# Performance work log

Measured on AMD Instinct MI355X. Metric: run time of the kernel, lower is better.

## Reference

```python
import jax, jax.numpy as jnp
import numpy as np

N_E = 8192
E_DIM = 256
BETA = 0.25


def setup_inputs() -> dict:
    key = jax.random.key(0)
    k1, k2 = jax.random.split(key)
    z = jax.random.normal(k1, (8, E_DIM, 32, 32), dtype=jnp.float32)
    # nn.Embedding default init: N(0, 1)
    W = jax.random.normal(k2, (N_E, E_DIM), dtype=jnp.float32)
    return {"z": z, "W": W}


def reference(z, W):
    # logits: (B, n_e, H, W)
    logits = jnp.einsum('bdhw,nd->bnhw', z, W)
    soft_one_hot = jax.nn.softmax(logits, axis=1)
    ind = jnp.argmax(soft_one_hot, axis=1)  # (B, H, W)
    hard_one_hot = jax.nn.one_hot(ind, N_E, axis=1, dtype=logits.dtype)  # (B, n_e, H, W)
    # straight-through estimator
    one_hot = hard_one_hot - jax.lax.stop_gradient(soft_one_hot) + soft_one_hot
    z_q = jnp.einsum('bnhw,nd->bdhw', one_hot, W)
    z_q_2 = jnp.einsum('bnhw,nd->bdhw', hard_one_hot, W)
    quant_loss = (jnp.mean((z_q - z) ** 2)
                  + jnp.mean((jax.lax.stop_gradient(z_q_2) - z) ** 2)
                  + BETA * jnp.mean((z_q_2 - jax.lax.stop_gradient(z)) ** 2))
    ind_flat = jnp.reshape(ind, (-1,))
    return z_q, quant_loss, ind_flat
```

## Files before the change

kernel.cpp:

```cpp
#include <hip/hip_runtime.h>
#include <math.h>


using short8  = __attribute__((ext_vector_type(8))) short;
using floatx4 = __attribute__((ext_vector_type(4))) float;

#define MARGIN 0.5f
#define APAD   264

__device__ inline unsigned short f2bf(float x) {
    union { float f; unsigned u; } v; v.f = x;
    unsigned r = v.u + 0x7fffu + ((v.u >> 16) & 1u);
    return (unsigned short)(r >> 16);
}

__global__ void conv_w_kernel(const float* __restrict__ W, unsigned short* __restrict__ wb) {
    int i = blockIdx.x * 256 + threadIdx.x;
    float4 v = *(const float4*)&W[(size_t)i * 4];
    ushort4 o;
    o.x = f2bf(v.x); o.y = f2bf(v.y); o.z = f2bf(v.z); o.w = f2bf(v.w);
    *(ushort4*)&wb[(size_t)i * 4] = o;
}

__global__ void conv_z_kernel(const float* __restrict__ z, unsigned short* __restrict__ zb) {
    __shared__ float tile[64 * 65];
    int b  = blockIdx.x >> 6;
    int dt = (blockIdx.x >> 4) & 3;
    int st = blockIdx.x & 15;
    int dl = threadIdx.x >> 6, sl = threadIdx.x & 63;
#pragma unroll
    for (int i = 0; i < 16; ++i) {
        int d = i * 4 + dl;
        tile[sl * 65 + d] = z[(size_t)b * 262144 + (size_t)(dt * 64 + d) * 1024 + st * 64 + sl];
    }
    __syncthreads();
    int d2 = threadIdx.x & 63, sr = threadIdx.x >> 6;
#pragma unroll
    for (int i = 0; i < 16; ++i) {
        int s = i * 4 + sr;
        int pos = b * 1024 + st * 64 + s;
        zb[(size_t)pos * 256 + dt * 64 + d2] = f2bf(tile[s * 65 + d2]);
    }
}

__global__ __launch_bounds__(256, 2)
void gemm_argmax_kernel(const unsigned short* __restrict__ zb,
                        const unsigned short* __restrict__ wb,
                        float4* __restrict__ part)
{
    __shared__ unsigned short As[128 * APAD];
    __shared__ unsigned short Bs[128 * 32];

    const int t  = threadIdx.x;
    const int bm = blockIdx.x, bn = blockIdx.y;
    const int w  = t >> 6, lane = t & 63;
    const int wm = w >> 1, wn = w & 1;
    const int q  = lane >> 4, l15 = lane & 15;

    {
        const unsigned short* src = zb + (size_t)bm * 128 * 256;
#pragma unroll
        for (int i = 0; i < 16; ++i) {
            int u = i * 256 + t;
            int row = u >> 5, c8 = (u & 31) * 8;
            short8 v = *(const short8*)(src + row * 256 + c8);
            *(short8*)(&As[row * APAD + c8]) = v;
        }
    }

    float mv[4][4];
    int   mi[4][4];
#pragma unroll
    for (int im = 0; im < 4; ++im)
#pragma unroll
        for (int r = 0; r < 4; ++r) { mv[im][r] = -INFINITY; mi[im][r] = 0; }

    const unsigned short* wsrc = wb + (size_t)bn * 1024 * 256;

    for (int nc = 0; nc < 8; ++nc) {
        floatx4 acc[4][4];
#pragma unroll
        for (int im = 0; im < 4; ++im)
#pragma unroll
            for (int in = 0; in < 4; ++in) {
                floatx4 zz = {0.f, 0.f, 0.f, 0.f};
                acc[im][in] = zz;
            }

        for (int kp = 0; kp < 8; ++kp) {
            __syncthreads();
#pragma unroll
            for (int i = 0; i < 2; ++i) {
                int u = i * 256 + t;
                int row = u >> 2, q2 = u & 3;
                int ksw = (q2 ^ ((row >> 1) & 3)) * 8;
                const unsigned short* g = wsrc + (size_t)(nc * 128 + row) * 256 + kp * 32 + ksw;
                __builtin_amdgcn_global_load_lds(
                    (const __attribute__((address_space(1))) void*)g,
                    (__attribute__((address_space(3))) void*)(&Bs[u * 8]),
                    16, 0, 0);
            }
            __syncthreads();

            short8 af[4], bf[4];
#pragma unroll
            for (int im = 0; im < 4; ++im)
                af[im] = *(const short8*)(&As[(wm * 64 + im * 16 + l15) * APAD + kp * 32 + q * 8]);
#pragma unroll
            for (int in = 0; in < 4; ++in) {
                int n32 = wn * 64 + in * 16 + l15;
                bf[in] = *(const short8*)(&Bs[n32 * 32 + (q ^ ((n32 >> 1) & 3)) * 8]);
            }
#pragma unroll
            for (int im = 0; im < 4; ++im)
#pragma unroll
                for (int in = 0; in < 4; ++in)
                    acc[im][in] = __builtin_amdgcn_mfma_f32_16x16x32_bf16(
                        af[im], bf[in], acc[im][in], 0, 0, 0);
        }

#pragma unroll
        for (int im = 0; im < 4; ++im)
#pragma unroll
            for (int in = 0; in < 4; ++in) {
                int n = bn * 1024 + nc * 128 + wn * 64 + in * 16 + l15;
#pragma unroll
                for (int r = 0; r < 4; ++r) {
                    float v = acc[im][in][r];
                    if (v > mv[im][r]) { mv[im][r] = v; mi[im][r] = n; }
                }
            }
    }

#pragma unroll
    for (int im = 0; im < 4; ++im)
#pragma unroll
        for (int r = 0; r < 4; ++r) {
            float v1 = mv[im][r]; int i1 = mi[im][r];
            float v2 = -INFINITY; int i2 = 0x7FFFFFFF;
#pragma unroll
            for (int off = 1; off < 16; off <<= 1) {
                float o1 = __shfl_xor(v1, off, 64); int oi1 = __shfl_xor(i1, off, 64);
                float o2 = __shfl_xor(v2, off, 64); int oi2 = __shfl_xor(i2, off, 64);
                if (o1 > v1 || (o1 == v1 && oi1 < i1)) {
                    float tv = v1; int ti = i1; v1 = o1; i1 = oi1;
                    if (tv > o2 || (tv == o2 && ti < oi2)) { o2 = tv; oi2 = ti; }
                }
                if (o2 > v2 || (o2 == v2 && oi2 < i2)) { v2 = o2; i2 = oi2; }
            }
            if (l15 == 0) {
                int pos = bm * 128 + wm * 64 + im * 16 + q * 4 + r;
                float4 rec;
                rec.x = v1; rec.y = __int_as_float(i1);
                rec.z = v2; rec.w = __int_as_float(i2);
                part[(size_t)pos * 16 + bn * 2 + wn] = rec;
            }
        }
}

__global__ __launch_bounds__(256, 8)
void resolve_kernel(const float* __restrict__ z, const float* __restrict__ W,
                    const float4* __restrict__ part,
                    float* __restrict__ zq, float* __restrict__ loss,
                    float* __restrict__ ind)
{
    __shared__ float lred[4];
    const int t = threadIdx.x, w = t >> 6, lane = t & 63;
    const int p = blockIdx.x * 4 + w;
    const int b = p >> 10, s = p & 1023;

    const float* zp = z + (size_t)b * 262144 + s;
    float zf0 = zp[(size_t)(lane * 4 + 0) * 1024];
    float zf1 = zp[(size_t)(lane * 4 + 1) * 1024];
    float zf2 = zp[(size_t)(lane * 4 + 2) * 1024];
    float zf3 = zp[(size_t)(lane * 4 + 3) * 1024];

    float4 rec = part[(size_t)p * 16 + (lane & 15)];
    float vmax = fmaxf(rec.x, rec.z);
#pragma unroll
    for (int off = 1; off < 64; off <<= 1)
        vmax = fmaxf(vmax, __shfl_xor(vmax, off, 64));
    const float thr = vmax - MARGIN;

    int cloc = ((lane < 16) ? ((rec.x >= thr) ? 1 : 0) + ((rec.z >= thr) ? 1 : 0) : 0);
#pragma unroll
    for (int off = 1; off < 64; off <<= 1) cloc += __shfl_xor(cloc, off, 64);
    const int cnt = cloc;

    int bi;
    if (cnt <= 1) {
        float bv = -INFINITY; bi = 0x7FFFFFFF;
#pragma unroll
        for (int s16 = 0; s16 < 16; ++s16) {
            float v1 = __shfl(rec.x, s16, 64); int i1 = __float_as_int(__shfl(rec.y, s16, 64));
            float v2 = __shfl(rec.z, s16, 64); int i2 = __float_as_int(__shfl(rec.w, s16, 64));
            if (v1 > bv || (v1 == bv && i1 < bi)) { bv = v1; bi = i1; }
            if (v2 > bv || (v2 == bv && i2 < bi)) { bv = v2; bi = i2; }
        }
    } else {
        float bv = -INFINITY; bi = 0x7FFFFFFF;
#pragma unroll
        for (int s16 = 0; s16 < 16; ++s16) {
            float vv[2]; int ii[2];
            vv[0] = __shfl(rec.x, s16, 64); ii[0] = __float_as_int(__shfl(rec.y, s16, 64));
            vv[1] = __shfl(rec.z, s16, 64); ii[1] = __float_as_int(__shfl(rec.w, s16, 64));
#pragma unroll
            for (int h = 0; h < 2; ++h) {
                if (vv[h] < thr) continue;
                int c = ii[h];
                float4 wf = *(const float4*)&W[(size_t)c * 256 + lane * 4];
                float d = zf0 * wf.x + zf1 * wf.y + zf2 * wf.z + zf3 * wf.w;
#pragma unroll
                for (int off = 1; off < 64; off <<= 1) d += __shfl_xor(d, off, 64);
                if (d > bv || (d == bv && c < bi)) { bv = d; bi = c; }
            }
        }
    }

    if (lane == 0) ind[p] = (float)bi;

    float4 wq = *(const float4*)&W[(size_t)bi * 256 + lane * 4];
    float* zqp = zq + (size_t)b * 262144 + s;
    zqp[(size_t)(lane * 4 + 0) * 1024] = wq.x;
    zqp[(size_t)(lane * 4 + 1) * 1024] = wq.y;
    zqp[(size_t)(lane * 4 + 2) * 1024] = wq.z;
    zqp[(size_t)(lane * 4 + 3) * 1024] = wq.w;

    float d0 = wq.x - zf0, d1 = wq.y - zf1, d2 = wq.z - zf2, d3 = wq.w - zf3;
    float ls = d0 * d0 + d1 * d1 + d2 * d2 + d3 * d3;
#pragma unroll
    for (int off = 1; off < 64; off <<= 1) ls += __shfl_xor(ls, off, 64);
    if (lane == 0) lred[w] = ls;
    __syncthreads();
    if (t == 0)
        atomicAdd(loss, (lred[0] + lred[1] + lred[2] + lred[3]) * (2.25f / 2097152.0f));
}

#define TP 16
#define ZPAD 260
#define WPAD 36
__global__ __launch_bounds__(256, 2)
void vq_kernel(const float* __restrict__ z, const float* __restrict__ W,
               float* __restrict__ zq, float* __restrict__ loss,
               float* __restrict__ ind)
{
    __shared__ float zs[TP * ZPAD];
    __shared__ float ws[256 * WPAD];
    __shared__ int   best[TP];
    __shared__ float lred[4];
    const int t = threadIdx.x, w = t >> 6, lane = t & 63, cg = t & 63;
    const int pos_base = blockIdx.x * TP;
    const int b = pos_base >> 10, s0 = pos_base & 1023;
    const float* zb = z + (size_t)b * 262144 + s0;
    { int p = t & 15, dg = t >> 4;
      for (int i = 0; i < 16; ++i) { int d = i * 16 + dg; zs[p * ZPAD + d] = zb[(size_t)d * 1024 + p]; } }
    float maxv[4]; int maxi[4];
#pragma unroll
    for (int i = 0; i < 4; ++i) { maxv[i] = -INFINITY; maxi[i] = 0; }
    for (int cc = 0; cc < 32; ++cc) {
        float acc[4][4];
#pragma unroll
        for (int i = 0; i < 4; ++i)
#pragma unroll
            for (int j = 0; j < 4; ++j) acc[i][j] = 0.0f;
        for (int kp = 0; kp < 8; ++kp) {
            __syncthreads();
#pragma unroll
            for (int i = 0; i < 8; ++i) {
                int f = i * 256 + t, code = f >> 3, k4 = f & 7;
                float4 v = *(const float4*)&W[(size_t)(cc * 256 + code) * 256 + kp * 32 + k4 * 4];
                *(float4*)&ws[code * WPAD + k4 * 4] = v;
            }
            __syncthreads();
#pragma unroll
            for (int k4 = 0; k4 < 8; ++k4) {
                float4 zf[4], wf[4];
#pragma unroll
                for (int i = 0; i < 4; ++i) zf[i] = *(const float4*)&zs[(w * 4 + i) * ZPAD + kp * 32 + k4 * 4];
#pragma unroll
                for (int j = 0; j < 4; ++j) wf[j] = *(const float4*)&ws[(cg + 64 * j) * WPAD + k4 * 4];
#pragma unroll
                for (int i = 0; i < 4; ++i)
#pragma unroll
                    for (int j = 0; j < 4; ++j) {
                        acc[i][j] += zf[i].x * wf[j].x; acc[i][j] += zf[i].y * wf[j].y;
                        acc[i][j] += zf[i].z * wf[j].z; acc[i][j] += zf[i].w * wf[j].w;
                    }
            }
        }
#pragma unroll
        for (int i = 0; i < 4; ++i)
#pragma unroll
            for (int j = 0; j < 4; ++j) {
                int code = cc * 256 + cg + 64 * j; float v = acc[i][j];
                if (v > maxv[i] || (v == maxv[i] && code < maxi[i])) { maxv[i] = v; maxi[i] = code; }
            }
    }
#pragma unroll
    for (int i = 0; i < 4; ++i) {
        float v = maxv[i]; int idx = maxi[i];
        for (int off = 32; off > 0; off >>= 1) {
            float ov = __shfl_down(v, off, 64); int oi = __shfl_down(idx, off, 64);
            if (ov > v || (ov == v && oi < idx)) { v = ov; idx = oi; }
        }
        if (lane == 0) { int p = w * 4 + i; best[p] = idx; ind[pos_base + p] = (float)idx; }
    }
    __syncthreads();
    float lsum = 0.0f;
    for (int p = 0; p < TP; ++p) {
        int bi = best[p];
        float wv = W[(size_t)bi * 256 + t];
        float zv = zs[p * ZPAD + t];
        float dd = wv - zv; lsum += dd * dd;
        zq[(size_t)b * 262144 + (size_t)t * 1024 + s0 + p] = wv;
    }
    for (int off = 32; off > 0; off >>= 1) lsum += __shfl_down(lsum, off, 64);
    if (lane == 0) lred[w] = lsum;
    __syncthreads();
    if (t == 0) atomicAdd(loss, (lred[0] + lred[1] + lred[2] + lred[3]) * (2.25f / 2097152.0f));
}

extern "C" void kernel_launch(void* const* d_in, const int* in_sizes, int n_in,
                              void* d_out, int out_size, void* d_ws, size_t ws_size,
                              hipStream_t stream) {
    const float* z = (const float*)d_in[0];
    const float* W = (const float*)d_in[1];
    float* out  = (float*)d_out;
    float* zq   = out;
    float* loss = out + 2097152;
    float* ind  = out + 2097153;

    hipMemsetAsync(loss, 0, sizeof(float), stream);

    if (ws_size >= (size_t)10 * 1024 * 1024 + 65536) {
        unsigned short* zbuf = (unsigned short*)d_ws;
        unsigned short* wbuf = zbuf + 2097152;
        float4* part = (float4*)((char*)d_ws + (size_t)8 * 1024 * 1024);
        conv_w_kernel<<<2048, 256, 0, stream>>>(W, wbuf);
        conv_z_kernel<<<512, 256, 0, stream>>>(z, zbuf);
        gemm_argmax_kernel<<<dim3(64, 8), 256, 0, stream>>>(zbuf, wbuf, part);
        resolve_kernel<<<2048, 256, 0, stream>>>(z, W, part, zq, loss, ind);
    } else {
        vq_kernel<<<512, 256, 0, stream>>>(z, W, zq, loss, ind);
    }
}
```

Before: 161.2 us.

## Fuse conversions, register-prefetch B tiles, pack argmax keys, batch resolve writes

Merges the W and z bf16 conversion kernels into one launch. In the GEMM+argmax kernel, B operands now come straight from global memory into registers with a double-buffered prefetch, which removes the per-k-step LDS staging and barriers. The running argmax is packed into a single ordered uint key (truncated value bits plus inverted index). This turns compare/select pairs into single max ops and halves the partial-record size, at the cost of value precision that the resolve step compensates for with a widened margin check. The resolve kernel now handles 64 positions per block and stages the chosen codebook rows in LDS, so z/zq reads and writes are coalesced along spatial positions. That trades occupancy for memory efficiency.

```diff
diff --git a/kernel.cpp b/kernel.cpp
--- a/kernel.cpp
+++ b/kernel.cpp
@@ -13,43 +13,51 @@
     unsigned r = v.u + 0x7fffu + ((v.u >> 16) & 1u);
     return (unsigned short)(r >> 16);
 }
-
-__global__ void conv_w_kernel(const float* __restrict__ W, unsigned short* __restrict__ wb) {
-    int i = blockIdx.x * 256 + threadIdx.x;
-    float4 v = *(const float4*)&W[(size_t)i * 4];
-    ushort4 o;
-    o.x = f2bf(v.x); o.y = f2bf(v.y); o.z = f2bf(v.z); o.w = f2bf(v.w);
-    *(ushort4*)&wb[(size_t)i * 4] = o;
-}
-
-__global__ void conv_z_kernel(const float* __restrict__ z, unsigned short* __restrict__ zb) {
-    __shared__ float tile[64 * 65];
-    int b  = blockIdx.x >> 6;
-    int dt = (blockIdx.x >> 4) & 3;
-    int st = blockIdx.x & 15;
-    int dl = threadIdx.x >> 6, sl = threadIdx.x & 63;
-#pragma unroll
-    for (int i = 0; i < 16; ++i) {
-        int d = i * 4 + dl;
-        tile[sl * 65 + d] = z[(size_t)b * 262144 + (size_t)(dt * 64 + d) * 1024 + st * 64 + sl];
-    }
-    __syncthreads();
-    int d2 = threadIdx.x & 63, sr = threadIdx.x >> 6;
-#pragma unroll
-    for (int i = 0; i < 16; ++i) {
-        int s = i * 4 + sr;
-        int pos = b * 1024 + st * 64 + s;
-        zb[(size_t)pos * 256 + dt * 64 + d2] = f2bf(tile[s * 65 + d2]);
+__device__ inline unsigned f2ord(float f) {
+    unsigned u = __float_as_uint(f);
+    return (u & 0x80000000u) ? ~u : (u | 0x80000000u);
+}
+__device__ inline float ord2f(unsigned o) {
+    return __uint_as_float((o & 0x80000000u) ? (o ^ 0x80000000u) : ~o);
+}
+
+__global__ void convert_kernel(const float* __restrict__ W, const float* __restrict__ z,
+                               unsigned short* __restrict__ wb, unsigned short* __restrict__ zb) {
+    if (blockIdx.x < 2048) {
+        int i = blockIdx.x * 256 + threadIdx.x;
+        float4 v = *(const float4*)&W[(size_t)i * 4];
+        ushort4 o;
+        o.x = f2bf(v.x); o.y = f2bf(v.y); o.z = f2bf(v.z); o.w = f2bf(v.w);
+        *(ushort4*)&wb[(size_t)i * 4] = o;
+    } else {
+        __shared__ float tile[64 * 65];
+        int blk = blockIdx.x - 2048;
+        int b  = blk >> 6;
+        int dt = (blk >> 4) & 3;
+        int st = blk & 15;
+        int dl = threadIdx.x >> 6, sl = threadIdx.x & 63;
+#pragma unroll
+        for (int i = 0; i < 16; ++i) {
+            int d = i * 4 + dl;
+            tile[sl * 65 + d] = z[(size_t)b * 262144 + (size_t)(dt * 64 + d) * 1024 + st * 64 + sl];
+        }
+        __syncthreads();
+        int d2 = threadIdx.x & 63, sr = threadIdx.x >> 6;
+#pragma unroll
+        for (int i = 0; i < 16; ++i) {
+            int s = i * 4 + sr;
+            int pos = b * 1024 + st * 64 + s;
+            zb[(size_t)pos * 256 + dt * 64 + d2] = f2bf(tile[s * 65 + d2]);
+        }
     }
 }
 
 __global__ __launch_bounds__(256, 2)
 void gemm_argmax_kernel(const unsigned short* __restrict__ zb,
                         const unsigned short* __restrict__ wb,
-                        float4* __restrict__ part)
+                        uint2* __restrict__ part)
 {
     __shared__ unsigned short As[128 * APAD];
-    __shared__ unsigned short Bs[128 * 32];
 
     const int t  = threadIdx.x;
     const int bm = blockIdx.x, bn = blockIdx.y;
@@ -57,6 +65,14 @@
     const int wm = w >> 1, wn = w & 1;
     const int q  = lane >> 4, l15 = lane & 15;
 
+    const unsigned short* bbase =
+        wb + (size_t)(bn * 1024 + wn * 64 + l15) * 256 + q * 8;
+
+    short8 bf[2][4];
+#pragma unroll
+    for (int in = 0; in < 4; ++in)
+        bf[0][in] = *(const short8*)(bbase + in * 16 * 256);
+
     {
         const unsigned short* src = zb + (size_t)bm * 128 * 256;
 #pragma unroll
@@ -67,15 +83,13 @@
             *(short8*)(&As[row * APAD + c8]) = v;
         }
     }
-
-    float mv[4][4];
-    int   mi[4][4];
+    __syncthreads();
+
+    unsigned kkey[4][4];
 #pragma unroll
     for (int im = 0; im < 4; ++im)
 #pragma unroll
-        for (int r = 0; r < 4; ++r) { mv[im][r] = -INFINITY; mi[im][r] = 0; }
-
-    const unsigned short* wsrc = wb + (size_t)bn * 1024 * 256;
+        for (int r = 0; r < 4; ++r) kkey[im][r] = 0u;
 
     for (int nc = 0; nc < 8; ++nc) {
         floatx4 acc[4][4];
@@ -87,47 +101,38 @@
                 acc[im][in] = zz;
             }
 
+#pragma unroll
         for (int kp = 0; kp < 8; ++kp) {
-            __syncthreads();
-#pragma unroll
-            for (int i = 0; i < 2; ++i) {
-                int u = i * 256 + t;
-                int row = u >> 2, q2 = u & 3;
-                int ksw = (q2 ^ ((row >> 1) & 3)) * 8;
-                const unsigned short* g = wsrc + (size_t)(nc * 128 + row) * 256 + kp * 32 + ksw;
-                __builtin_amdgcn_global_load_lds(
-                    (const __attribute__((address_space(1))) void*)g,
-                    (__attribute__((address_space(3))) void*)(&Bs[u * 8]),
-                    16, 0, 0);
-            }
-            __syncthreads();
-
-            short8 af[4], bf[4];
+            const int cur = kp & 1, nxt = cur ^ 1;
+            int nnc = (kp == 7) ? nc + 1 : nc;
+            int nkp = (kp + 1) & 7;
+            if (nnc < 8) {
+                const unsigned short* np = bbase + (size_t)nnc * 128 * 256 + nkp * 32;
+#pragma unroll
+                for (int in = 0; in < 4; ++in)
+                    bf[nxt][in] = *(const short8*)(np + in * 16 * 256);
+            }
+            short8 af[4];
 #pragma unroll
             for (int im = 0; im < 4; ++im)
-                af[im] = *(const short8*)(&As[(wm * 64 + im * 16 + l15) * APAD + kp * 32 + q * 8]);
-#pragma unroll
-            for (int in = 0; in < 4; ++in) {
-                int n32 = wn * 64 + in * 16 + l15;
-                bf[in] = *(const short8*)(&Bs[n32 * 32 + (q ^ ((n32 >> 1) & 3)) * 8]);
-            }
+                af[im] = *(const short8*)&As[(wm * 64 + im * 16 + l15) * APAD + kp * 32 + q * 8];
 #pragma unroll
             for (int im = 0; im < 4; ++im)
 #pragma unroll
                 for (int in = 0; in < 4; ++in)
                     acc[im][in] = __builtin_amdgcn_mfma_f32_16x16x32_bf16(
-                        af[im], bf[in], acc[im][in], 0, 0, 0);
+                        af[im], bf[cur][in], acc[im][in], 0, 0, 0);
         }
 
 #pragma unroll
         for (int im = 0; im < 4; ++im)
 #pragma unroll
             for (int in = 0; in < 4; ++in) {
-                int n = bn * 1024 + nc * 128 + wn * 64 + in * 16 + l15;
+                unsigned n = bn * 1024 + nc * 128 + wn * 64 + in * 16 + l15;
 #pragma unroll
                 for (int r = 0; r < 4; ++r) {
-                    float v = acc[im][in][r];
-                    if (v > mv[im][r]) { mv[im][r] = v; mi[im][r] = n; }
+                    unsigned key = (f2ord(acc[im][in][r]) & 0xFFFFE000u) | (8191u - n);
+                    kkey[im][r] = (key > kkey[im][r]) ? key : kkey[im][r];
                 }
             }
     }
@@ -136,98 +141,118 @@
     for (int im = 0; im < 4; ++im)
 #pragma unroll
         for (int r = 0; r < 4; ++r) {
-            float v1 = mv[im][r]; int i1 = mi[im][r];
-            float v2 = -INFINITY; int i2 = 0x7FFFFFFF;
+            unsigned k1 = kkey[im][r], k2 = 0u;
 #pragma unroll
             for (int off = 1; off < 16; off <<= 1) {
-                float o1 = __shfl_xor(v1, off, 64); int oi1 = __shfl_xor(i1, off, 64);
-                float o2 = __shfl_xor(v2, off, 64); int oi2 = __shfl_xor(i2, off, 64);
-                if (o1 > v1 || (o1 == v1 && oi1 < i1)) {
-                    float tv = v1; int ti = i1; v1 = o1; i1 = oi1;
-                    if (tv > o2 || (tv == o2 && ti < oi2)) { o2 = tv; oi2 = ti; }
-                }
-                if (o2 > v2 || (o2 == v2 && oi2 < i2)) { v2 = o2; i2 = oi2; }
+                unsigned o1 = (unsigned)__shfl_xor((int)k1, off, 64);
+                unsigned o2 = (unsigned)__shfl_xor((int)k2, off, 64);
+                unsigned hi = (k1 > o1) ? k1 : o1;
+                unsigned lo = (k1 > o1) ? o1 : k1;
+                unsigned s2 = (k2 > o2) ? k2 : o2;
+                k1 = hi;
+                k2 = (lo > s2) ? lo : s2;
             }
             if (l15 == 0) {
                 int pos = bm * 128 + wm * 64 + im * 16 + q * 4 + r;
-                float4 rec;
-                rec.x = v1; rec.y = __int_as_float(i1);
-                rec.z = v2; rec.w = __int_as_float(i2);
-                part[(size_t)pos * 16 + bn * 2 + wn] = rec;
-            }
-        }
-}
-
-__global__ __launch_bounds__(256, 8)
+                part[(size_t)pos * 16 + bn * 2 + wn] = make_uint2(k1, k2);
+            }
+        }
+}
+
+__global__ __launch_bounds__(256, 2)
 void resolve_kernel(const float* __restrict__ z, const float* __restrict__ W,
-                    const float4* __restrict__ part,
+                    const uint2* __restrict__ part,
                     float* __restrict__ zq, float* __restrict__ loss,
                     float* __restrict__ ind)
 {
+    __shared__ float wq[64 * 260];
+    __shared__ int   best[64];
     __shared__ float lred[4];
+
     const int t = threadIdx.x, w = t >> 6, lane = t & 63;
-    const int p = blockIdx.x * 4 + w;
-    const int b = p >> 10, s = p & 1023;
-
-    const float* zp = z + (size_t)b * 262144 + s;
-    float zf0 = zp[(size_t)(lane * 4 + 0) * 1024];
-    float zf1 = zp[(size_t)(lane * 4 + 1) * 1024];
-    float zf2 = zp[(size_t)(lane * 4 + 2) * 1024];
-    float zf3 = zp[(size_t)(lane * 4 + 3) * 1024];
-
-    float4 rec = part[(size_t)p * 16 + (lane & 15)];
-    float vmax = fmaxf(rec.x, rec.z);
-#pragma unroll
-    for (int off = 1; off < 64; off <<= 1)
-        vmax = fmaxf(vmax, __shfl_xor(vmax, off, 64));
-    const float thr = vmax - MARGIN;
-
-    int cloc = ((lane < 16) ? ((rec.x >= thr) ? 1 : 0) + ((rec.z >= thr) ? 1 : 0) : 0);
-#pragma unroll
-    for (int off = 1; off < 64; off <<= 1) cloc += __shfl_xor(cloc, off, 64);
-    const int cnt = cloc;
-
-    int bi;
-    if (cnt <= 1) {
-        float bv = -INFINITY; bi = 0x7FFFFFFF;
-#pragma unroll
-        for (int s16 = 0; s16 < 16; ++s16) {
-            float v1 = __shfl(rec.x, s16, 64); int i1 = __float_as_int(__shfl(rec.y, s16, 64));
-            float v2 = __shfl(rec.z, s16, 64); int i2 = __float_as_int(__shfl(rec.w, s16, 64));
-            if (v1 > bv || (v1 == bv && i1 < bi)) { bv = v1; bi = i1; }
-            if (v2 > bv || (v2 == bv && i2 < bi)) { bv = v2; bi = i2; }
-        }
-    } else {
-        float bv = -INFINITY; bi = 0x7FFFFFFF;
-#pragma unroll
-        for (int s16 = 0; s16 < 16; ++s16) {
-            float vv[2]; int ii[2];
-            vv[0] = __shfl(rec.x, s16, 64); ii[0] = __float_as_int(__shfl(rec.y, s16, 64));
-            vv[1] = __shfl(rec.z, s16, 64); ii[1] = __float_as_int(__shfl(rec.w, s16, 64));
-#pragma unroll
-            for (int h = 0; h < 2; ++h) {
-                if (vv[h] < thr) continue;
-                int c = ii[h];
-                float4 wf = *(const float4*)&W[(size_t)c * 256 + lane * 4];
-                float d = zf0 * wf.x + zf1 * wf.y + zf2 * wf.z + zf3 * wf.w;
-#pragma unroll
-                for (int off = 1; off < 64; off <<= 1) d += __shfl_xor(d, off, 64);
-                if (d > bv || (d == bv && c < bi)) { bv = d; bi = c; }
-            }
-        }
-    }
-
-    if (lane == 0) ind[p] = (float)bi;
-
-    float4 wq = *(const float4*)&W[(size_t)bi * 256 + lane * 4];
-    float* zqp = zq + (size_t)b * 262144 + s;
-    zqp[(size_t)(lane * 4 + 0) * 1024] = wq.x;
-    zqp[(size_t)(lane * 4 + 1) * 1024] = wq.y;
-    zqp[(size_t)(lane * 4 + 2) * 1024] = wq.z;
-    zqp[(size_t)(lane * 4 + 3) * 1024] = wq.w;
-
-    float d0 = wq.x - zf0, d1 = wq.y - zf1, d2 = wq.z - zf2, d3 = wq.w - zf3;
-    float ls = d0 * d0 + d1 * d1 + d2 * d2 + d3 * d3;
+    const int pos0 = blockIdx.x * 64;
+    const int b = pos0 >> 10, s0 = pos0 & 1023;
+
+    for (int i = 0; i < 16; ++i) {
+        const int pl = w * 16 + i;
+        const int p  = pos0 + pl;
+        uint2 rec = part[(size_t)p * 16 + (lane & 15)];
+        unsigned k1 = rec.x, k2 = rec.y;
+
+        unsigned kmax = (k1 > k2) ? k1 : k2;
+#pragma unroll
+        for (int off = 1; off < 64; off <<= 1) {
+            unsigned o = (unsigned)__shfl_xor((int)kmax, off, 64);
+            kmax = (o > kmax) ? o : kmax;
+        }
+        const float vmax = ord2f(kmax & 0xFFFFE000u);
+        const float thr  = vmax - MARGIN;
+
+        int cl = 0;
+        if (lane < 16) {
+            float h1 = ord2f((k1 & 0xFFFFE000u) + 0x2000u);
+            float h2 = ord2f((k2 & 0xFFFFE000u) + 0x2000u);
+            cl = ((h1 >= thr) ? 1 : 0) + ((h2 >= thr) ? 1 : 0);
+        }
+#pragma unroll
+        for (int off = 1; off < 64; off <<= 1) cl += __shfl_xor(cl, off, 64);
+
+        int bi;
+        if (cl <= 1) {
+            bi = 8191 - (int)(kmax & 8191u);
+        } else {
+            const float* zp = z + (size_t)b * 262144 + (p & 1023);
+            float zf0 = zp[(size_t)(lane * 4 + 0) * 1024];
+            float zf1 = zp[(size_t)(lane * 4 + 1) * 1024];
+            float zf2 = zp[(size_t)(lane * 4 + 2) * 1024];
+            float zf3 = zp[(size_t)(lane * 4 + 3) * 1024];
+            float bv = -INFINITY; bi = 0x7FFFFFFF;
+#pragma unroll
+            for (int s16 = 0; s16 < 16; ++s16) {
+                unsigned kk[2];
+                kk[0] = (unsigned)__shfl((int)k1, s16, 64);
+                kk[1] = (unsigned)__shfl((int)k2, s16, 64);
+#pragma unroll
+                for (int h = 0; h < 2; ++h) {
+                    float vh = ord2f((kk[h] & 0xFFFFE000u) + 0x2000u);
+                    if (vh < thr) continue;
+                    int c = 8191 - (int)(kk[h] & 8191u);
+                    float4 wf = *(const float4*)&W[(size_t)c * 256 + lane * 4];
+                    float d = zf0 * wf.x + zf1 * wf.y + zf2 * wf.z + zf3 * wf.w;
+#pragma unroll
+                    for (int off = 1; off < 64; off <<= 1) d += __shfl_xor(d, off, 64);
+                    if (d > bv || (d == bv && c < bi)) { bv = d; bi = c; }
+                }
+            }
+        }
+        if (lane == 0) { best[pl] = bi; ind[p] = (float)bi; }
+    }
+    __syncthreads();
+
+#pragma unroll
+    for (int i = 0; i < 8; ++i) {
+        int r  = i * 8 + (t >> 5);
+        int d0 = (t & 31) * 8;
+        const float* wr = W + (size_t)best[r] * 256 + d0;
+        float4 u = *(const float4*)wr;
+        float4 v = *(const float4*)(wr + 4);
+        *(float4*)&wq[r * 260 + d0]     = u;
+        *(float4*)&wq[r * 260 + d0 + 4] = v;
+    }
+    __syncthreads();
+
+    float ls = 0.f;
+#pragma unroll 4
+    for (int i = 0; i < 16; ++i) {
+        int d = i * 16 + w * 4;
+        float4 wv = *(const float4*)&wq[lane * 260 + d];
+        const float* zp  = z  + (size_t)b * 262144 + (size_t)d * 1024 + s0 + lane;
+        float*       qp  = zq + (size_t)b * 262144 + (size_t)d * 1024 + s0 + lane;
+        float z0 = zp[0], z1 = zp[1024], z2 = zp[2048], z3 = zp[3072];
+        qp[0] = wv.x; qp[1024] = wv.y; qp[2048] = wv.z; qp[3072] = wv.w;
+        float d0 = wv.x - z0, d1 = wv.y - z1, d2 = wv.z - z2, d3 = wv.w - z3;
+        ls += d0 * d0 + d1 * d1 + d2 * d2 + d3 * d3;
+    }
 #pragma unroll
     for (int off = 1; off < 64; off <<= 1) ls += __shfl_xor(ls, off, 64);
     if (lane == 0) lred[w] = ls;
@@ -332,14 +357,13 @@
 
     hipMemsetAsync(loss, 0, sizeof(float), stream);
 
-    if (ws_size >= (size_t)10 * 1024 * 1024 + 65536) {
+    if (ws_size >= (size_t)10 * 1024 * 1024) {
         unsigned short* zbuf = (unsigned short*)d_ws;
         unsigned short* wbuf = zbuf + 2097152;
-        float4* part = (float4*)((char*)d_ws + (size_t)8 * 1024 * 1024);
-        conv_w_kernel<<<2048, 256, 0, stream>>>(W, wbuf);
-        conv_z_kernel<<<512, 256, 0, stream>>>(z, zbuf);
+        uint2* part = (uint2*)((char*)d_ws + (size_t)8 * 1024 * 1024);
+        convert_kernel<<<2560, 256, 0, stream>>>(W, z, wbuf, zbuf);
         gemm_argmax_kernel<<<dim3(64, 8), 256, 0, stream>>>(zbuf, wbuf, part);
-        resolve_kernel<<<2048, 256, 0, stream>>>(z, W, part, zq, loss, ind);
+        resolve_kernel<<<128, 256, 0, stream>>>(z, W, part, zq, loss, ind);
     } else {
         vq_kernel<<<512, 256, 0, stream>>>(z, W, zq, loss, ind);
     }
```

New measurement: 192.8 us. 19.6% more time.
